# Optimization experiments

Measured on AMD Instinct MI355X. Metric: run time of the kernel, lower is better.

## Reference

```python
import jax, jax.numpy as jnp
import numpy as np

N, E, G = 10000, 160000, 64      # nodes, edges, graphs
IN, H, L = 128, 128, 14          # in_channels, hidden, num GENConv layers
EPS_LN = 1e-5                    # torch LayerNorm eps
EPS_MSG = 1e-7                   # GENConv message eps


def layer_norm(x, g, b):
    mu = jnp.mean(x, axis=-1, keepdims=True)
    v = jnp.var(x, axis=-1, keepdims=True)
    return (x - mu) * jax.lax.rsqrt(v + EPS_LN) * g + b


def gen_conv(h, src, dst, t, sc, W1, b1, mg, mb, W2, b2):
    # message: relu(x_j) + eps  (no edge_attr)
    msg = jax.nn.relu(h[src]) + EPS_MSG                      # [E, H]
    # softmax aggregation over edges sharing a destination, per feature
    z = msg * t
    mx = jax.ops.segment_max(z, dst, num_segments=N)         # [N, H]
    mx = jnp.where(jnp.isfinite(mx), mx, 0.0)
    e = jnp.exp(z - mx[dst])
    ssum = jax.ops.segment_sum(e, dst, num_segments=N)
    alpha = e / (ssum[dst] + 1e-16)
    agg = jax.ops.segment_sum(msg * alpha, dst, num_segments=N)  # [N, H]
    # MessageNorm: normalize(agg) * ||h|| * scale
    agg = agg / jnp.maximum(jnp.linalg.norm(agg, axis=-1, keepdims=True), 1e-12)
    agg = agg * jnp.linalg.norm(h, axis=-1, keepdims=True) * sc
    out = h + agg
    # MLP [H, 2H, H] with LayerNorm + ReLU between (dropout off in eval)
    z1 = layer_norm(out @ W1 + b1, mg, mb)
    return jax.nn.relu(z1) @ W2 + b2


def setup_inputs() -> dict:
    key = jax.random.key(0)
    ks = jax.random.split(key, 8)
    s = 0.05
    x = jax.random.normal(ks[0], (N, IN), jnp.float32)
    edge_index = jax.random.randint(ks[1], (2, E), 0, N, dtype=jnp.int64)
    batch = jnp.sort(jax.random.randint(ks[2], (N,), 0, G, dtype=jnp.int64))
    enc_W = jax.random.normal(ks[3], (IN, H), jnp.float32) * s
    enc_b = jnp.zeros((H,), jnp.float32)
    ln_g = jnp.ones((L, H), jnp.float32)
    ln_b = jnp.zeros((L, H), jnp.float32)
    t = jnp.ones((L,), jnp.float32)         # learnable softmax temperature
    scale = jnp.ones((L,), jnp.float32)     # learnable MsgNorm scale
    W1 = jax.random.normal(ks[4], (L, H, 2 * H), jnp.float32) * s
    b1 = jnp.zeros((L, 2 * H), jnp.float32)
    mg = jnp.ones((L, 2 * H), jnp.float32)
    mb = jnp.zeros((L, 2 * H), jnp.float32)
    W2 = jax.random.normal(ks[5], (L, 2 * H, H), jnp.float32) * s
    b2 = jnp.zeros((L, H), jnp.float32)
    fn_g = jnp.ones((H,), jnp.float32)
    fn_b = jnp.zeros((H,), jnp.float32)
    return dict(x=x, edge_index=edge_index, batch=batch, enc_W=enc_W, enc_b=enc_b,
                ln_g=ln_g, ln_b=ln_b, t=t, scale=scale, W1=W1, b1=b1, mg=mg, mb=mb,
                W2=W2, b2=b2, fn_g=fn_g, fn_b=fn_b)


def reference(x, edge_index, batch, enc_W, enc_b, ln_g, ln_b, t, scale,
              W1, b1, mg, mb, W2, b2, fn_g, fn_b):
    src, dst = edge_index[0], edge_index[1]
    h = x @ enc_W + enc_b
    for i in range(L):  # DeepGCNLayer 'res+': x + conv(act(norm(x)))
        r = jax.nn.leaky_relu(layer_norm(h, ln_g[i], ln_b[i]), 0.01)
        h = h + gen_conv(r, src, dst, t[i], scale[i],
                         W1[i], b1[i], mg[i], mb[i], W2[i], b2[i])
    h = jax.nn.leaky_relu(layer_norm(h, fn_g, fn_b), 0.01)
    # global_mean_pool (fin_map is unused in the original forward)
    cnt = jax.ops.segment_sum(jnp.ones((N,), h.dtype), batch, num_segments=G)
    gf = jax.ops.segment_sum(h, batch, num_segments=G) / jnp.maximum(cnt, 1.0)[:, None]
    return gf
```

## Files before the change

### kernel.cpp

```cpp
#include <hip/hip_runtime.h>
#include <cstdint>
#include <cstddef>


#define BT 512

typedef __attribute__((ext_vector_type(8))) short bf16x8;
typedef __attribute__((ext_vector_type(4))) float f32x4;

__device__ inline float bf2f(ushort u) {
    union { uint i; float f; } v;
    v.i = (uint)u << 16;
    return v.f;
}
__device__ inline ushort f2bf(float f) {
    union { float f; uint i; } v;
    v.f = f;
    return (ushort)((v.i + 0x7fffu + ((v.i >> 16) & 1u)) >> 16);
}
__device__ inline uint f2bf2(float a, float b) {
    return (uint)f2bf(a) | ((uint)f2bf(b) << 16);
}
__device__ inline float fast_exp2(float x) {
    return __builtin_amdgcn_exp2f(x);
}

__global__ void setup_kernel(const float* __restrict__ x, ushort* __restrict__ xb,
                             const int* __restrict__ dst, int* __restrict__ deg,
                             const int* __restrict__ batch, int* __restrict__ gstart,
                             int total, int N, int E, int G) {
    int idx = blockIdx.x * blockDim.x + threadIdx.x;
    if (idx >= total) return;
    xb[idx] = f2bf(x[idx]);
    if (idx < E) atomicAdd(&deg[dst[idx]], 1);
    if (idx < N) {
        int bb = batch[idx];
        if (idx == 0)
            for (int g = 0; g <= bb; g++) gstart[g] = 0;
        else {
            int pb = batch[idx - 1];
            for (int g = pb + 1; g <= bb; g++) gstart[g] = idx;
        }
        if (idx == N - 1)
            for (int g = bb + 1; g <= G; g++) gstart[g] = N;
    }
}

__global__ __launch_bounds__(1024) void scan_kernel(const int* __restrict__ deg,
                                                    int* __restrict__ offs,
                                                    int* __restrict__ cursor, int N) {
    __shared__ int part[1024];
    int tid = threadIdx.x;
    int CH = (N + 1023) / 1024;
    int base = tid * CH;
    int s = 0;
    for (int i = 0; i < CH; i++) {
        int idx = base + i;
        if (idx < N) s += deg[idx];
    }
    part[tid] = s;
    __syncthreads();
    for (int off = 1; off < 1024; off <<= 1) {
        int v = (tid >= off) ? part[tid - off] : 0;
        __syncthreads();
        part[tid] += v;
        __syncthreads();
    }
    int run = (tid == 0) ? 0 : part[tid - 1];
    for (int i = 0; i < CH; i++) {
        int idx = base + i;
        if (idx < N) {
            offs[idx] = run;
            cursor[idx] = run;
            run += deg[idx];
        }
    }
    if (tid == 1023) offs[N] = part[1023];
}

__global__ void scatter_kernel(const int* __restrict__ src, const int* __restrict__ dst,
                               int* __restrict__ cursor, int* __restrict__ esrc, int E) {
    int e = blockIdx.x * blockDim.x + threadIdx.x;
    if (e < E) {
        int d = dst[e];
        int pos = atomicAdd(&cursor[d], 1);
        esrc[pos] = src[e];
    }
}

__global__ __launch_bounds__(1024) void sort_kernel(const int* __restrict__ offs,
                                                    int* __restrict__ perm, int N) {
    __shared__ int hist[256];
    __shared__ int cur[256];
    int tid = threadIdx.x;
    if (tid < 256) hist[tid] = 0;
    __syncthreads();
    for (int n = tid; n < N; n += 1024) {
        int d = offs[n + 1] - offs[n];
        int key = 255 - min(d, 255);
        atomicAdd(&hist[key], 1);
    }
    __syncthreads();
    if (tid == 0) {
        int run = 0;
        for (int i = 0; i < 256; i++) {
            cur[i] = run;
            run += hist[i];
        }
    }
    __syncthreads();
    for (int n = tid; n < N; n += 1024) {
        int d = offs[n + 1] - offs[n];
        int key = 255 - min(d, 255);
        int pos = atomicAdd(&cur[key], 1);
        perm[pos] = n;
    }
}

__global__ __launch_bounds__(256) void prep_kernel(const float* __restrict__ W1,
                                                   const float* __restrict__ W2,
                                                   const float* __restrict__ encW,
                                                   ushort* __restrict__ W1t,
                                                   ushort* __restrict__ W2t,
                                                   ushort* __restrict__ encWt, int L) {
    __shared__ float tile[32][33];
    int z = blockIdx.z;
    const float* in;
    ushort* out;
    int R, C;
    if (z < L) {
        in = W1 + (size_t)z * 32768; out = W1t + (size_t)z * 32768; R = 128; C = 256;
    } else if (z < 2 * L) {
        int i = z - L;
        in = W2 + (size_t)i * 32768; out = W2t + (size_t)i * 32768; R = 256; C = 128;
    } else {
        in = encW; out = encWt; R = 128; C = 128;
    }
    int r0 = blockIdx.y * 32, c0 = blockIdx.x * 32;
    if (r0 >= R || c0 >= C) return;
    int tx = threadIdx.x & 31, ty = threadIdx.x >> 5;
    for (int i = ty; i < 32; i += 8) tile[i][tx] = in[(size_t)(r0 + i) * C + c0 + tx];
    __syncthreads();
    for (int i = ty; i < 32; i += 8)
        out[(size_t)(c0 + i) * R + r0 + tx] = f2bf(tile[tx][i]);
}

__device__ __forceinline__ void agg_stage(const ushort* __restrict__ rin,
                                          const int* __restrict__ offs,
                                          const int* __restrict__ esrc,
                                          const float* __restrict__ rnbuf,
                                          float tv2, float sv,
                                          int nd0, int nd1,
                                          int w, int l, uint (*AsU)[68]) {
    const uint2* rin2 = (const uint2*)rin;
    int half = l >> 5, li = l & 31;
    int eb[2], dg[2];
    eb[0] = offs[nd0]; dg[0] = offs[nd0 + 1] - eb[0];
    eb[1] = offs[nd1]; dg[1] = offs[nd1 + 1] - eb[1];

    uint2 ru0 = rin2[(size_t)nd0 * 32 + li];
    uint2 ru1 = rin2[(size_t)nd1 * 32 + li];
    float rn0 = rnbuf[nd0], rn1 = rnbuf[nd1];

    float s[2][4] = {}, W[2][4] = {};
    int mxdeg = max(dg[0], dg[1]);

#pragma unroll 1
    for (int base = 0; base < mxdeg; base += 64) {
        int rem0 = min(dg[0] - base, 64);
        int rem1 = min(dg[1] - base, 64);
        int idx0 = (rem0 > 0 && l < rem0) ? esrc[eb[0] + base + l] : 0;
        int idx1 = (rem1 > 0 && l < rem1) ? esrc[eb[1] + base + l] : 0;
        int it = (max(rem0, rem1) + 7) >> 3;
#pragma unroll 1
        for (int i = 0; i < it; i++) {
            int j0 = i * 8 + half;
            uint2 rv[2][4];
            bool vl[2][4];
#pragma unroll
            for (int c = 0; c < 4; c++) {
                int j = j0 + 2 * c;
                vl[0][c] = j < rem0;
                vl[1][c] = j < rem1;
                int sn0 = __shfl(idx0, j, 64);
                int sn1 = __shfl(idx1, j, 64);
                if (vl[0][c]) rv[0][c] = rin2[(size_t)sn0 * 32 + li];
                if (vl[1][c]) rv[1][c] = rin2[(size_t)sn1 * 32 + li];
            }
#pragma unroll
            for (int k = 0; k < 2; k++)
#pragma unroll
                for (int c = 0; c < 4; c++) {
                    if (vl[k][c]) {
                        float f0 = bf2f((ushort)(rv[k][c].x & 0xffff));
                        float f1 = bf2f((ushort)(rv[k][c].x >> 16));
                        float f2 = bf2f((ushort)(rv[k][c].y & 0xffff));
                        float f3 = bf2f((ushort)(rv[k][c].y >> 16));
                        float g0 = fmaxf(f0, 0.f) + 1e-7f;
                        float g1 = fmaxf(f1, 0.f) + 1e-7f;
                        float g2 = fmaxf(f2, 0.f) + 1e-7f;
                        float g3 = fmaxf(f3, 0.f) + 1e-7f;
                        float p0 = fast_exp2(g0 * tv2);
                        float p1 = fast_exp2(g1 * tv2);
                        float p2 = fast_exp2(g2 * tv2);
                        float p3 = fast_exp2(g3 * tv2);
                        s[k][0] += p0; W[k][0] += g0 * p0;
                        s[k][1] += p1; W[k][1] += g1 * p1;
                        s[k][2] += p2; W[k][2] += g2 * p2;
                        s[k][3] += p3; W[k][3] += g3 * p3;
                    }
                }
        }
    }

#pragma unroll
    for (int k = 0; k < 2; k++) {
#pragma unroll
        for (int f = 0; f < 4; f++) {
            s[k][f] += __shfl_xor(s[k][f], 32, 64);
            W[k][f] += __shfl_xor(W[k][f], 32, 64);
        }
        float agg[4], nsq = 0.f;
#pragma unroll
        for (int f = 0; f < 4; f++) {
            agg[f] = W[k][f] / (s[k][f] + 1e-16f);
            nsq += agg[f] * agg[f];
        }
#pragma unroll
        for (int off = 1; off < 32; off <<= 1) nsq += __shfl_xor(nsq, off, 64);
        float rnv = (k == 0) ? rn0 : rn1;
        uint2 ru = (k == 0) ? ru0 : ru1;
        float fac = rnv * sv / fmaxf(sqrtf(nsq), 1e-12f);
        if (half == 0) {
            uint2 o;
            o.x = f2bf2(bf2f((ushort)(ru.x & 0xffff)) + agg[0] * fac,
                        bf2f((ushort)(ru.x >> 16)) + agg[1] * fac);
            o.y = f2bf2(bf2f((ushort)(ru.y & 0xffff)) + agg[2] * fac,
                        bf2f((ushort)(ru.y >> 16)) + agg[3] * fac);
            *(uint2*)&AsU[2 * w + k][2 * li] = o;
        }
    }
}

__device__ __forceinline__ void gemm1_stage8(const ushort (*As)[136],
                                             const ushort* __restrict__ Bt,
                                             const float* __restrict__ bias,
                                             const float* __restrict__ mg,
                                             const float* __restrict__ mb,
                                             ushort (*z1s)[264],
                                             int w, int q, int ln,
                                             float (*pS)[16], float (*pQ)[16]) {
    f32x4 acc[2];
    acc[0] = (f32x4){0.f, 0.f, 0.f, 0.f};
    acc[1] = (f32x4){0.f, 0.f, 0.f, 0.f};
#pragma unroll
    for (int ks = 0; ks < 128; ks += 32) {
        bf16x8 a = *(const bf16x8*)&As[ln][ks + q * 8];
#pragma unroll
        for (int ct = 0; ct < 2; ct++) {
            bf16x8 bv = *(const bf16x8*)(Bt + (size_t)(w * 32 + ct * 16 + ln) * 128 + ks + q * 8);
            acc[ct] = __builtin_amdgcn_mfma_f32_16x16x32_bf16(a, bv, acc[ct], 0, 0, 0);
        }
    }
    float s1[4] = {0, 0, 0, 0}, s2[4] = {0, 0, 0, 0};
#pragma unroll
    for (int ct = 0; ct < 2; ct++)
#pragma unroll
        for (int r = 0; r < 4; r++) {
            float v = acc[ct][r] + bias[w * 32 + ct * 16 + ln];
            acc[ct][r] = v;
            s1[r] += v;
            s2[r] += v * v;
        }
#pragma unroll
    for (int off = 1; off < 16; off <<= 1)
#pragma unroll
        for (int r = 0; r < 4; r++) {
            s1[r] += __shfl_xor(s1[r], off, 64);
            s2[r] += __shfl_xor(s2[r], off, 64);
        }
    if (ln == 0)
#pragma unroll
        for (int r = 0; r < 4; r++) {
            pS[w][q * 4 + r] = s1[r];
            pQ[w][q * 4 + r] = s2[r];
        }
    __syncthreads();
#pragma unroll
    for (int r = 0; r < 4; r++) {
        int row = q * 4 + r;
        float S = 0.f, Q = 0.f;
#pragma unroll
        for (int ww = 0; ww < 8; ww++) {
            S += pS[ww][row];
            Q += pQ[ww][row];
        }
        float mu = S * (1.f / 256.f);
        float var = Q * (1.f / 256.f) - mu * mu;
        float rs = rsqrtf(var + 1e-5f);
#pragma unroll
        for (int ct = 0; ct < 2; ct++) {
            int col = w * 32 + ct * 16 + ln;
            float y = (acc[ct][r] - mu) * rs * mg[col] + mb[col];
            z1s[row][col] = f2bf(fmaxf(y, 0.f));
        }
    }
    __syncthreads();
}

template <int KD, bool RESID>
__device__ __forceinline__ void out_stage8(const ushort* __restrict__ Abase, int astr,
                                           const ushort* __restrict__ Bt,
                                           const float* __restrict__ bias,
                                           const float* __restrict__ lg,
                                           const float* __restrict__ lb,
                                           ushort* __restrict__ hbuf,
                                           ushort* __restrict__ rout,
                                           float* __restrict__ rnbuf,
                                           const int* rowmap,
                                           int w, int q, int ln,
                                           float (*pS)[16], float (*pQ)[16]) {
    f32x4 acc = (f32x4){0.f, 0.f, 0.f, 0.f};
    int col = w * 16 + ln;
#pragma unroll
    for (int ks = 0; ks < KD; ks += 32) {
        bf16x8 a = *(const bf16x8*)(Abase + ln * astr + ks + q * 8);
        bf16x8 bv = *(const bf16x8*)(Bt + (size_t)col * KD + ks + q * 8);
        acc = __builtin_amdgcn_mfma_f32_16x16x32_bf16(a, bv, acc, 0, 0, 0);
    }
    float s1[4], s2[4];
#pragma unroll
    for (int r = 0; r < 4; r++) {
        int grow = rowmap[q * 4 + r];
        float v = acc[r] + bias[col];
        if (RESID) v += bf2f(hbuf[(size_t)grow * 128 + col]);
        hbuf[(size_t)grow * 128 + col] = f2bf(v);
        acc[r] = v;
        s1[r] = v;
        s2[r] = v * v;
    }
#pragma unroll
    for (int off = 1; off < 16; off <<= 1)
#pragma unroll
        for (int r = 0; r < 4; r++) {
            s1[r] += __shfl_xor(s1[r], off, 64);
            s2[r] += __shfl_xor(s2[r], off, 64);
        }
    if (ln == 0)
#pragma unroll
        for (int r = 0; r < 4; r++) {
            pS[w][q * 4 + r] = s1[r];
            pQ[w][q * 4 + r] = s2[r];
        }
    __syncthreads();
    float yv[4];
    float t2[4];
#pragma unroll
    for (int r = 0; r < 4; r++) {
        int row = q * 4 + r;
        float S = 0.f, Q = 0.f;
#pragma unroll
        for (int ww = 0; ww < 8; ww++) {
            S += pS[ww][row];
            Q += pQ[ww][row];
        }
        float mu = S * (1.f / 128.f);
        float var = Q * (1.f / 128.f) - mu * mu;
        float rs = rsqrtf(var + 1e-5f);
        float y = (acc[r] - mu) * rs * lg[col] + lb[col];
        y = y > 0.f ? y : 0.01f * y;
        yv[r] = y;
        t2[r] = y * y;
    }
#pragma unroll
    for (int off = 1; off < 16; off <<= 1)
#pragma unroll
        for (int r = 0; r < 4; r++) t2[r] += __shfl_xor(t2[r], off, 64);
    __syncthreads();
    if (ln == 0)
#pragma unroll
        for (int r = 0; r < 4; r++) pS[w][q * 4 + r] = t2[r];
    __syncthreads();
#pragma unroll
    for (int r = 0; r < 4; r++) {
        int grow = rowmap[q * 4 + r];
        float T = 0.f;
#pragma unroll
        for (int ww = 0; ww < 8; ww++) T += pS[ww][q * 4 + r];
        if (w == 0 && ln == 0) rnbuf[grow] = sqrtf(T);
        rout[(size_t)grow * 128 + col] = f2bf(yv[r]);
    }
}

__global__ __launch_bounds__(BT) void enc_kernel(const ushort* __restrict__ xb,
                                                 const ushort* __restrict__ encWt,
                                                 const float* __restrict__ encB,
                                                 const float* __restrict__ lg,
                                                 const float* __restrict__ lb,
                                                 ushort* __restrict__ h,
                                                 ushort* __restrict__ rbuf,
                                                 float* __restrict__ rn, int N) {
    __shared__ __align__(16) ushort As[16][136];
    __shared__ float pS[8][16], pQ[8][16];
    __shared__ int rowmap[16];
    uint(*AsU)[68] = (uint(*)[68])As;
    int tid = threadIdx.x, w = tid >> 6, l = tid & 63;
    int q = l >> 4, ln = l & 15;
    int row0 = blockIdx.x * 16;
    if (tid < 16) rowmap[tid] = row0 + tid;
    for (int idx = tid; idx < 16 * 64; idx += BT) {
        int row = idx >> 6, cl = idx & 63;
        AsU[row][cl] = ((const uint*)xb)[(size_t)(row0 + row) * 64 + cl];
    }
    __syncthreads();
    out_stage8<128, false>(&As[0][0], 136, encWt, encB, lg, lb, h, rbuf, rn,
                           rowmap, w, q, ln, pS, pQ);
}

__global__ __launch_bounds__(BT) void layer_kernel(const ushort* __restrict__ rin,
                                                   ushort* __restrict__ rout,
                                                   const int* __restrict__ offs,
                                                   const int* __restrict__ esrc,
                                                   const int* __restrict__ perm,
                                                   float* __restrict__ rn,
                                                   ushort* __restrict__ h,
                                                   const ushort* __restrict__ W1t,
                                                   const ushort* __restrict__ W2t,
                                                   const float* __restrict__ b1,
                                                   const float* __restrict__ mg,
                                                   const float* __restrict__ mb,
                                                   const float* __restrict__ b2,
                                                   const float* __restrict__ ng,
                                                   const float* __restrict__ nb,
                                                   const float* __restrict__ tptr,
                                                   const float* __restrict__ scptr,
                                                   int N) {
    __shared__ __align__(16) ushort As[16][136];
    __shared__ __align__(16) ushort z1s[16][264];
    __shared__ float pS[8][16], pQ[8][16];
    __shared__ int rowmap[16];
    uint(*AsU)[68] = (uint(*)[68])As;
    int tid = threadIdx.x, w = tid >> 6, l = tid & 63;
    int q = l >> 4, ln = l & 15;
    int row0 = blockIdx.x * 16;
    if (tid < 16) rowmap[tid] = perm[row0 + tid];
    __syncthreads();
    float tv2 = (*tptr) * 1.4426950408889634f;
    float sv = *scptr;
    agg_stage(rin, offs, esrc, rn, tv2, sv,
              rowmap[2 * w], rowmap[2 * w + 1], w, l, AsU);
    __syncthreads();
    gemm1_stage8(As, W1t, b1, mg, mb, z1s, w, q, ln, pS, pQ);
    out_stage8<256, true>(&z1s[0][0], 264, W2t, b2, ng, nb, h, rout, rn,
                          rowmap, w, q, ln, pS, pQ);
}

__global__ __launch_bounds__(256) void pool_kernel(const ushort* __restrict__ rf,
                                                   const int* __restrict__ gstart,
                                                   float* __restrict__ out) {
    __shared__ float pb0[4][64], pb1[4][64];
    int g = blockIdx.x;
    int w = threadIdx.x >> 6, l = threadIdx.x & 63;
    int s = gstart[g], e = gstart[g + 1];
    float a0 = 0.f, a1 = 0.f;
    for (int n = s + w; n < e; n += 4) {
        uint rv = ((const uint*)rf)[(size_t)n * 64 + l];
        a0 += bf2f((ushort)(rv & 0xffff));
        a1 += bf2f((ushort)(rv >> 16));
    }
    pb0[w][l] = a0;
    pb1[w][l] = a1;
    __syncthreads();
    if (threadIdx.x < 64) {
        float t0 = pb0[0][l] + pb0[1][l] + pb0[2][l] + pb0[3][l];
        float t1 = pb1[0][l] + pb1[1][l] + pb1[2][l] + pb1[3][l];
        float inv = 1.f / fmaxf((float)(e - s), 1.f);
        out[g * 128 + 2 * l] = t0 * inv;
        out[g * 128 + 2 * l + 1] = t1 * inv;
    }
}

extern "C" void kernel_launch(void* const* d_in, const int* in_sizes, int n_in,
                              void* d_out, int out_size, void* d_ws, size_t ws_size,
                              hipStream_t stream) {
    const float* x     = (const float*)d_in[0];
    const int*   ei    = (const int*)d_in[1];
    const int*   batch = (const int*)d_in[2];
    const float* encW  = (const float*)d_in[3];
    const float* encB  = (const float*)d_in[4];
    const float* ln_g  = (const float*)d_in[5];
    const float* ln_b  = (const float*)d_in[6];
    const float* tArr  = (const float*)d_in[7];
    const float* scArr = (const float*)d_in[8];
    const float* W1    = (const float*)d_in[9];
    const float* b1    = (const float*)d_in[10];
    const float* mg    = (const float*)d_in[11];
    const float* mb    = (const float*)d_in[12];
    const float* W2    = (const float*)d_in[13];
    const float* b2    = (const float*)d_in[14];
    const float* fn_g  = (const float*)d_in[15];
    const float* fn_b  = (const float*)d_in[16];
    float* out = (float*)d_out;

    const int N = in_sizes[0] / 128;
    const int E = in_sizes[1] / 2;
    const int L = in_sizes[7];
    const int G = 64;

    const int* src = ei;
    const int* dst = ei + E;

    char* p = (char*)d_ws;
    auto alloc = [&](size_t bytes) -> void* {
        void* qp = (void*)p;
        p += (bytes + 255) & ~(size_t)255;
        return qp;
    };
    int*    deg    = (int*)alloc((size_t)N * 4);
    int*    offs   = (int*)alloc((size_t)(N + 1) * 4);
    int*    cursor = (int*)alloc((size_t)N * 4);
    int*    esrc   = (int*)alloc((size_t)E * 4);
    int*    gstart = (int*)alloc((size_t)(G + 1) * 4);
    int*    perm   = (int*)alloc((size_t)N * 4);
    ushort* h      = (ushort*)alloc((size_t)N * 128 * 2);
    ushort* r0     = (ushort*)alloc((size_t)N * 128 * 2);
    ushort* r1     = (ushort*)alloc((size_t)N * 128 * 2);
    float*  rn     = (float*)alloc((size_t)N * 4);
    ushort* xb     = (ushort*)alloc((size_t)N * 128 * 2);
    ushort* W1t    = (ushort*)alloc((size_t)L * 32768 * 2);
    ushort* W2t    = (ushort*)alloc((size_t)L * 32768 * 2);
    ushort* encWt  = (ushort*)alloc((size_t)16384 * 2);

    (void)hipMemsetAsync(deg, 0, (size_t)N * 4, stream);

    setup_kernel<<<(N * 128 + 255) / 256, 256, 0, stream>>>(x, xb, dst, deg, batch,
                                                            gstart, N * 128, N, E, G);
    scan_kernel<<<1, 1024, 0, stream>>>(deg, offs, cursor, N);
    scatter_kernel<<<(E + 255) / 256, 256, 0, stream>>>(src, dst, cursor, esrc, E);
    sort_kernel<<<1, 1024, 0, stream>>>(offs, perm, N);
    prep_kernel<<<dim3(8, 8, 2 * L + 1), 256, 0, stream>>>(W1, W2, encW, W1t, W2t,
                                                           encWt, L);

    const int TILES = N / 16;

    enc_kernel<<<TILES, BT, 0, stream>>>(xb, encWt, encB, ln_g, ln_b, h, r0, rn, N);

    for (int i = 0; i < L; i++) {
        const ushort* rin = (i & 1) ? r1 : r0;
        ushort* rout = (i & 1) ? r0 : r1;
        const float* ng = (i < L - 1) ? (ln_g + (size_t)(i + 1) * 128) : fn_g;
        const float* nb = (i < L - 1) ? (ln_b + (size_t)(i + 1) * 128) : fn_b;
        layer_kernel<<<TILES, BT, 0, stream>>>(rin, rout, offs, esrc, perm, rn, h,
                                               W1t + ((size_t)i << 15),
                                               W2t + ((size_t)i << 15),
                                               b1 + (size_t)i * 256,
                                               mg + (size_t)i * 256,
                                               mb + (size_t)i * 256,
                                               b2 + (size_t)i * 128,
                                               ng, nb, tArr + i, scArr + i, N);
    }

    const ushort* rf = ((L - 1) & 1) ? r0 : r1;
    pool_kernel<<<G, 256, 0, stream>>>(rf, gstart, out);
}
```

Baseline: 570.4 us.

## Prefetch neighbor rows in aggregation, merge scatter/sort launches, drop a barrier

The aggregation loop now software-pipelines the gathered neighbor rows: the next batch of eight rows is loaded before the current batch is processed, and index loads are clamped so they need no predicate. The scatter and degree-sort kernels are merged into one launch, with the last block doing the sort. A separate shared buffer for the row-norm partial sums lets one __syncthreads be removed. These target gather latency and launch overhead, at the cost of more registers and possibly lower occupancy.

```diff
diff --git a/kernel.cpp b/kernel.cpp
--- a/kernel.cpp
+++ b/kernel.cpp
@@ -78,21 +78,25 @@
     if (tid == 1023) offs[N] = part[1023];
 }
 
-__global__ void scatter_kernel(const int* __restrict__ src, const int* __restrict__ dst,
-                               int* __restrict__ cursor, int* __restrict__ esrc, int E) {
-    int e = blockIdx.x * blockDim.x + threadIdx.x;
-    if (e < E) {
-        int d = dst[e];
-        int pos = atomicAdd(&cursor[d], 1);
-        esrc[pos] = src[e];
-    }
-}
-
-__global__ __launch_bounds__(1024) void sort_kernel(const int* __restrict__ offs,
-                                                    int* __restrict__ perm, int N) {
+__global__ __launch_bounds__(1024) void scatter_sort_kernel(const int* __restrict__ src,
+                                                            const int* __restrict__ dst,
+                                                            int* __restrict__ cursor,
+                                                            int* __restrict__ esrc,
+                                                            const int* __restrict__ offs,
+                                                            int* __restrict__ perm,
+                                                            int E, int N, int SB) {
+    int b = blockIdx.x, tid = threadIdx.x;
+    if (b < SB) {
+        int e = b * 1024 + tid;
+        if (e < E) {
+            int d = dst[e];
+            int pos = atomicAdd(&cursor[d], 1);
+            esrc[pos] = src[e];
+        }
+        return;
+    }
     __shared__ int hist[256];
     __shared__ int cur[256];
-    int tid = threadIdx.x;
     if (tid < 256) hist[tid] = 0;
     __syncthreads();
     for (int n = tid; n < N; n += 1024) {
@@ -154,44 +158,57 @@
                                           int w, int l, uint (*AsU)[68]) {
     const uint2* rin2 = (const uint2*)rin;
     int half = l >> 5, li = l & 31;
-    int eb[2], dg[2];
-    eb[0] = offs[nd0]; dg[0] = offs[nd0 + 1] - eb[0];
-    eb[1] = offs[nd1]; dg[1] = offs[nd1 + 1] - eb[1];
+    int eb0 = offs[nd0], dg0 = offs[nd0 + 1] - eb0;
+    int eb1 = offs[nd1], dg1 = offs[nd1 + 1] - eb1;
 
     uint2 ru0 = rin2[(size_t)nd0 * 32 + li];
     uint2 ru1 = rin2[(size_t)nd1 * 32 + li];
     float rn0 = rnbuf[nd0], rn1 = rnbuf[nd1];
 
     float s[2][4] = {}, W[2][4] = {};
-    int mxdeg = max(dg[0], dg[1]);
+    int mxdeg = max(dg0, dg1);
 
 #pragma unroll 1
     for (int base = 0; base < mxdeg; base += 64) {
-        int rem0 = min(dg[0] - base, 64);
-        int rem1 = min(dg[1] - base, 64);
-        int idx0 = (rem0 > 0 && l < rem0) ? esrc[eb[0] + base + l] : 0;
-        int idx1 = (rem1 > 0 && l < rem1) ? esrc[eb[1] + base + l] : 0;
+        int rem0 = min(dg0 - base, 64);
+        int rem1 = min(dg1 - base, 64);
+        int idx0 = esrc[eb0 + base + min(l, max(rem0 - 1, 0))];
+        int idx1 = esrc[eb1 + base + min(l, max(rem1 - 1, 0))];
         int it = (max(rem0, rem1) + 7) >> 3;
+
+        uint2 rv[2][4], rvn[2][4];
+        {
+            int j0 = half;
+#pragma unroll
+            for (int c = 0; c < 4; c++) {
+                int j = min(j0 + 2 * c, 63);
+                int sn0 = __shfl(idx0, j, 64);
+                int sn1 = __shfl(idx1, j, 64);
+                rv[0][c] = rin2[(size_t)sn0 * 32 + li];
+                rv[1][c] = rin2[(size_t)sn1 * 32 + li];
+            }
+        }
 #pragma unroll 1
         for (int i = 0; i < it; i++) {
+            if (i + 1 < it) {
+                int j0 = (i + 1) * 8 + half;
+#pragma unroll
+                for (int c = 0; c < 4; c++) {
+                    int j = min(j0 + 2 * c, 63);
+                    int sn0 = __shfl(idx0, j, 64);
+                    int sn1 = __shfl(idx1, j, 64);
+                    rvn[0][c] = rin2[(size_t)sn0 * 32 + li];
+                    rvn[1][c] = rin2[(size_t)sn1 * 32 + li];
+                }
+            }
             int j0 = i * 8 + half;
-            uint2 rv[2][4];
-            bool vl[2][4];
-#pragma unroll
-            for (int c = 0; c < 4; c++) {
-                int j = j0 + 2 * c;
-                vl[0][c] = j < rem0;
-                vl[1][c] = j < rem1;
-                int sn0 = __shfl(idx0, j, 64);
-                int sn1 = __shfl(idx1, j, 64);
-                if (vl[0][c]) rv[0][c] = rin2[(size_t)sn0 * 32 + li];
-                if (vl[1][c]) rv[1][c] = rin2[(size_t)sn1 * 32 + li];
-            }
-#pragma unroll
-            for (int k = 0; k < 2; k++)
+#pragma unroll
+            for (int k = 0; k < 2; k++) {
+                int rem = (k == 0) ? rem0 : rem1;
 #pragma unroll
                 for (int c = 0; c < 4; c++) {
-                    if (vl[k][c]) {
+                    bool vl = (j0 + 2 * c) < rem;
+                    if (vl) {
                         float f0 = bf2f((ushort)(rv[k][c].x & 0xffff));
                         float f1 = bf2f((ushort)(rv[k][c].x >> 16));
                         float f2 = bf2f((ushort)(rv[k][c].y & 0xffff));
@@ -210,6 +227,11 @@
                         s[k][3] += p3; W[k][3] += g3 * p3;
                     }
                 }
+            }
+#pragma unroll
+            for (int k = 0; k < 2; k++)
+#pragma unroll
+                for (int c = 0; c < 4; c++) rv[k][c] = rvn[k][c];
         }
     }
 
@@ -319,7 +341,8 @@
                                            float* __restrict__ rnbuf,
                                            const int* rowmap,
                                            int w, int q, int ln,
-                                           float (*pS)[16], float (*pQ)[16]) {
+                                           float (*pS)[16], float (*pQ)[16],
+                                           float (*pT)[16]) {
     f32x4 acc = (f32x4){0.f, 0.f, 0.f, 0.f};
     int col = w * 16 + ln;
 #pragma unroll
@@ -376,17 +399,16 @@
     for (int off = 1; off < 16; off <<= 1)
 #pragma unroll
         for (int r = 0; r < 4; r++) t2[r] += __shfl_xor(t2[r], off, 64);
-    __syncthreads();
     if (ln == 0)
 #pragma unroll
-        for (int r = 0; r < 4; r++) pS[w][q * 4 + r] = t2[r];
+        for (int r = 0; r < 4; r++) pT[w][q * 4 + r] = t2[r];
     __syncthreads();
 #pragma unroll
     for (int r = 0; r < 4; r++) {
         int grow = rowmap[q * 4 + r];
         float T = 0.f;
 #pragma unroll
-        for (int ww = 0; ww < 8; ww++) T += pS[ww][q * 4 + r];
+        for (int ww = 0; ww < 8; ww++) T += pT[ww][q * 4 + r];
         if (w == 0 && ln == 0) rnbuf[grow] = sqrtf(T);
         rout[(size_t)grow * 128 + col] = f2bf(yv[r]);
     }
@@ -401,7 +423,7 @@
                                                  ushort* __restrict__ rbuf,
                                                  float* __restrict__ rn, int N) {
     __shared__ __align__(16) ushort As[16][136];
-    __shared__ float pS[8][16], pQ[8][16];
+    __shared__ float pS[8][16], pQ[8][16], pT[8][16];
     __shared__ int rowmap[16];
     uint(*AsU)[68] = (uint(*)[68])As;
     int tid = threadIdx.x, w = tid >> 6, l = tid & 63;
@@ -414,7 +436,7 @@
     }
     __syncthreads();
     out_stage8<128, false>(&As[0][0], 136, encWt, encB, lg, lb, h, rbuf, rn,
-                           rowmap, w, q, ln, pS, pQ);
+                           rowmap, w, q, ln, pS, pQ, pT);
 }
 
 __global__ __launch_bounds__(BT) void layer_kernel(const ushort* __restrict__ rin,
@@ -437,7 +459,7 @@
                                                    int N) {
     __shared__ __align__(16) ushort As[16][136];
     __shared__ __align__(16) ushort z1s[16][264];
-    __shared__ float pS[8][16], pQ[8][16];
+    __shared__ float pS[8][16], pQ[8][16], pT[8][16];
     __shared__ int rowmap[16];
     uint(*AsU)[68] = (uint(*)[68])As;
     int tid = threadIdx.x, w = tid >> 6, l = tid & 63;
@@ -452,7 +474,7 @@
     __syncthreads();
     gemm1_stage8(As, W1t, b1, mg, mb, z1s, w, q, ln, pS, pQ);
     out_stage8<256, true>(&z1s[0][0], 264, W2t, b2, ng, nb, h, rout, rn,
-                          rowmap, w, q, ln, pS, pQ);
+                          rowmap, w, q, ln, pS, pQ, pT);
 }
 
 __global__ __launch_bounds__(256) void pool_kernel(const ushort* __restrict__ rf,
@@ -536,8 +558,9 @@
     setup_kernel<<<(N * 128 + 255) / 256, 256, 0, stream>>>(x, xb, dst, deg, batch,
                                                             gstart, N * 128, N, E, G);
     scan_kernel<<<1, 1024, 0, stream>>>(deg, offs, cursor, N);
-    scatter_kernel<<<(E + 255) / 256, 256, 0, stream>>>(src, dst, cursor, esrc, E);
-    sort_kernel<<<1, 1024, 0, stream>>>(offs, perm, N);
+    const int SB = (E + 1023) / 1024;
+    scatter_sort_kernel<<<SB + 1, 1024, 0, stream>>>(src, dst, cursor, esrc,
+                                                     offs, perm, E, N, SB);
     prep_kernel<<<dim3(8, 8, 2 * L + 1), 256, 0, stream>>>(W1, W2, encW, W1t, W2t,
                                                            encWt, L);
 
```

Result: slower. 625.5 us (+9.7%).
